# Performance work log

Measured on AMD Instinct MI355X. Metric: run time of the kernel, lower is better.

Reference implementation:

```python
import jax, jax.numpy as jnp
import numpy as np

C_IN = 128
C_HID = 32
N_HEADS = 4
INF = 1000000000.0


def setup_inputs() -> dict:
    key = jax.random.key(0)
    ks = jax.random.split(key, 12)
    B, I, J = 1, 256, 256
    hc = N_HEADS * C_HID
    s = 0.02
    return {
        "x": jax.random.normal(ks[0], (B, I, J, C_IN), dtype=jnp.float32),
        "mask": jnp.ones((B, I, J), dtype=jnp.float32),
        "ln_w": jnp.ones((C_IN,), dtype=jnp.float32),
        "ln_b": jnp.zeros((C_IN,), dtype=jnp.float32),
        "w_tri": jax.random.normal(ks[1], (C_IN, N_HEADS), dtype=jnp.float32) * s,
        "wq": jax.random.normal(ks[2], (C_IN, hc), dtype=jnp.float32) * s,
        "wk": jax.random.normal(ks[3], (C_IN, hc), dtype=jnp.float32) * s,
        "wv": jax.random.normal(ks[4], (C_IN, hc), dtype=jnp.float32) * s,
        "wg": jax.random.normal(ks[5], (C_IN, hc), dtype=jnp.float32) * s,
        "bg": jnp.ones((hc,), dtype=jnp.float32),
        "wo": jax.random.normal(ks[6], (hc, C_IN), dtype=jnp.float32) * s,
        "bo": jnp.zeros((C_IN,), dtype=jnp.float32),
    }


def _layer_norm(x, w, b, eps=1e-5):
    mu = jnp.mean(x, axis=-1, keepdims=True)
    var = jnp.var(x, axis=-1, keepdims=True)
    return (x - mu) * jax.lax.rsqrt(var + eps) * w + b


def _triangle_attention(x, mask, ln_w, ln_b, w_tri, wq, wk, wv, wg, bg, wo, bo):
    # starting=True: no transpose. x: [B, I, J, C]
    B, I, J, C = x.shape
    x = _layer_norm(x, ln_w, ln_b)
    # mask_bias: [B, I, 1, 1, J]
    mask_bias = (INF * (mask - 1.0))[..., :, None, None, :]
    # triangle_bias: linear(x) -> [B, I, J, H], permute (2,0,1) -> [B, H, I, J], unsqueeze -> [B, 1, H, I, J]
    tri = jnp.einsum("bijc,ch->bhij", x, w_tri)[:, None]  # [B, 1, H, I, J]
    # q/k/v: [B, I, H, J, Ch]
    def proj(w):
        return jnp.einsum("bijc,c(" + "" + ")->bijc", x, w) if False else (
            (x @ w).reshape(B, I, J, N_HEADS, C_HID).transpose(0, 1, 3, 2, 4))
    q = proj(wq) * (C_HID ** -0.5)
    k = proj(wk)
    v = proj(wv)
    # scores: [B, I, H, J, J]; biases broadcast over H (mask_bias) / I (tri over b,1 dim matches i? no)
    scores = jnp.einsum("bihqc,bihkc->bihqk", q, k)
    scores = scores + mask_bias + tri  # tri [B,1,H,I,J] broadcasts: i-dim aligns with query? matches torch broadcast [B,I,H,J,J]+[B,1,H,J,J]... wait tri is [B,1,H,I,J] with I==J so it broadcasts over the batch-of-rows dim
    a = jax.nn.softmax(scores, axis=-1)
    o = jnp.einsum("bihqk,bihkc->bihqc", a, v)  # [B, I, H, J, Ch]
    o = o.transpose(0, 1, 3, 2, 4).reshape(B, I, J, N_HEADS * C_HID)
    g = jax.nn.sigmoid(x @ wg + bg)
    o = o * g
    return o @ wo + bo  # [B, I, J, C]


def reference(x, mask, ln_w, ln_b, w_tri, wq, wk, wv, wg, bg, wo, bo):
    return _triangle_attention(x, mask, ln_w, ln_b, w_tri, wq, wk, wv, wg, bg, wo, bo)
```

## Files before the change

kernel.cpp:

```cpp
#include <hip/hip_runtime.h>


typedef __attribute__((ext_vector_type(4))) float f32x4;
typedef __attribute__((ext_vector_type(8))) short bf16x8;
#define MFMA16(a, b, c) __builtin_amdgcn_mfma_f32_16x16x32_bf16(a, b, c, 0, 0, 0)
#define LOG2E 1.4426950408889634f

__device__ __forceinline__ float bf2f(unsigned int u16) {
    return __uint_as_float(u16 << 16);
}
__device__ __forceinline__ unsigned int f2bf(float f) {
    unsigned int u = __float_as_uint(f);
    return (u + 0x7fffu + ((u >> 16) & 1u)) >> 16;
}
__device__ __forceinline__ unsigned int pack2(float a, float b) {
    return f2bf(a) | (f2bf(b) << 16);
}
__device__ __forceinline__ unsigned int cvt_pk_bf16(float lo, float hi) {
    unsigned int r;
    asm("v_cvt_pk_bf16_f32 %0, %1, %2" : "=v"(r) : "v"(lo), "v"(hi));
    return r;
}

__global__ __launch_bounds__(128) void k_prep(
    const float* __restrict__ wq, const float* __restrict__ wk,
    const float* __restrict__ wv, const float* __restrict__ wg,
    const float* __restrict__ wo, unsigned short* __restrict__ wT)
{
    const int mat = blockIdx.x, k0 = blockIdx.y * 16, t = threadIdx.x;
    const float* W = (mat == 0) ? wq : (mat == 1) ? wk : (mat == 2) ? wv
                     : (mat == 3) ? wg : wo;
    unsigned short* T = wT + mat * 16384;
    float col[16];
    #pragma unroll
    for (int kk = 0; kk < 16; ++kk) col[kk] = W[(k0 + kk) * 128 + t];
    unsigned int pk[8];
    #pragma unroll
    for (int u = 0; u < 8; ++u) pk[u] = pack2(col[2 * u], col[2 * u + 1]);
    *(uint4*)(T + t * 128 + k0)     = make_uint4(pk[0], pk[1], pk[2], pk[3]);
    *(uint4*)(T + t * 128 + k0 + 8) = make_uint4(pk[4], pk[5], pk[6], pk[7]);
}

__global__ __launch_bounds__(256, 2) void k_lnproj(
    const float* __restrict__ x, const float* __restrict__ ln_w,
    const float* __restrict__ ln_b, const float* __restrict__ w_tri,
    const unsigned short* __restrict__ wT, const float* __restrict__ bg,
    unsigned short* __restrict__ qb, unsigned short* __restrict__ kb,
    unsigned short* __restrict__ vtb, unsigned short* __restrict__ gb,
    float* __restrict__ triT)
{
    __shared__ unsigned short sA[128 * 136];
    __shared__ unsigned short sB[128 * 136];
    __shared__ unsigned short sWt[16 * 136];

    const int t = threadIdx.x, w = t >> 6, lane = t & 63;
    const int l15 = lane & 15, g = lane >> 4;
    const int rowBase = blockIdx.x * 128;

    if (t < 128) {
        const float4 wv = ((const float4*)w_tri)[t];
        sWt[0 * 136 + t] = (unsigned short)f2bf(wv.x);
        sWt[1 * 136 + t] = (unsigned short)f2bf(wv.y);
        sWt[2 * 136 + t] = (unsigned short)f2bf(wv.z);
        sWt[3 * 136 + t] = (unsigned short)f2bf(wv.w);
    } else {
        #pragma unroll
        for (int u = 0; u < 13; ++u) {
            const int idx = (t - 128) + 128 * u;
            if (idx < 12 * 136) sWt[4 * 136 + idx] = 0;
        }
    }

    {
        const int r = t >> 1, half = t & 1;
        const float* xr = x + (size_t)(rowBase + r) * 128 + half * 64;
        float v[64];
        float s1 = 0.0f, s2 = 0.0f;
        #pragma unroll
        for (int u = 0; u < 16; ++u) {
            const float4 q4 = ((const float4*)xr)[u];
            v[4*u] = q4.x; v[4*u+1] = q4.y; v[4*u+2] = q4.z; v[4*u+3] = q4.w;
            s1 += q4.x + q4.y + q4.z + q4.w;
            s2 += q4.x*q4.x + q4.y*q4.y + q4.z*q4.z + q4.w*q4.w;
        }
        s1 += __shfl_xor(s1, 1);
        s2 += __shfl_xor(s2, 1);
        const float mu = s1 * (1.0f / 128.0f);
        const float rs = rsqrtf(s2 * (1.0f / 128.0f) - mu * mu + 1e-5f);
        const float4* lw = (const float4*)(ln_w + half * 64);
        const float4* lb = (const float4*)(ln_b + half * 64);
        #pragma unroll
        for (int u = 0; u < 16; ++u) {
            const float4 w4 = lw[u], b4 = lb[u];
            v[4*u]   = (v[4*u]   - mu) * rs * w4.x + b4.x;
            v[4*u+1] = (v[4*u+1] - mu) * rs * w4.y + b4.y;
            v[4*u+2] = (v[4*u+2] - mu) * rs * w4.z + b4.z;
            v[4*u+3] = (v[4*u+3] - mu) * rs * w4.w + b4.w;
        }
        #pragma unroll
        for (int u = 0; u < 8; ++u) {
            uint4 pk;
            pk.x = pack2(v[8*u],   v[8*u+1]);
            pk.y = pack2(v[8*u+2], v[8*u+3]);
            pk.z = pack2(v[8*u+4], v[8*u+5]);
            pk.w = pack2(v[8*u+6], v[8*u+7]);
            *(uint4*)&sA[r * 136 + half * 64 + u * 8] = pk;
        }
    }
    __syncthreads();

    bf16x8 af[2][4];
    #pragma unroll
    for (int m = 0; m < 2; ++m)
        #pragma unroll
        for (int ks = 0; ks < 4; ++ks)
            af[m][ks] = *(const bf16x8*)&sA[(w * 32 + m * 16 + l15) * 136 + ks * 32 + g * 8];

    #pragma unroll
    for (int m = 0; m < 2; ++m) {
        f32x4 tc = (f32x4){0.f, 0.f, 0.f, 0.f};
        #pragma unroll
        for (int ks = 0; ks < 4; ++ks) {
            const bf16x8 bfw = *(const bf16x8*)&sWt[l15 * 136 + ks * 32 + g * 8];
            tc = MFMA16(af[m][ks], bfw, tc);
        }
        if (l15 < 4) {
            #pragma unroll
            for (int reg = 0; reg < 4; ++reg) {
                const int gr = rowBase + w * 32 + m * 16 + 4 * g + reg;
                triT[l15 * 65536 + gr] = tc[reg] * LOG2E;
            }
        }
    }

    const int r2 = t >> 1, half2 = t & 1;
    for (int mat = 0; mat < 4; ++mat) {
        {
            const unsigned short* Wm = wT + mat * 16384 + r2 * 128 + half2 * 64;
            #pragma unroll
            for (int u = 0; u < 8; ++u)
                *(uint4*)&sB[r2 * 136 + half2 * 64 + u * 8] = *(const uint4*)(Wm + u * 8);
        }
        __syncthreads();

        f32x4 acc[2][8];
        #pragma unroll
        for (int m = 0; m < 2; ++m)
            #pragma unroll
            for (int n = 0; n < 8; ++n) acc[m][n] = (f32x4){0.f, 0.f, 0.f, 0.f};
        #pragma unroll
        for (int n = 0; n < 8; ++n)
            #pragma unroll
            for (int ks = 0; ks < 4; ++ks) {
                const bf16x8 bf = *(const bf16x8*)&sB[(n * 16 + l15) * 136 + ks * 32 + g * 8];
                acc[0][n] = MFMA16(af[0][ks], bf, acc[0][n]);
                acc[1][n] = MFMA16(af[1][ks], bf, acc[1][n]);
            }
        __syncthreads();

        float bgv[8];
        if (mat == 3) {
            #pragma unroll
            for (int n = 0; n < 8; ++n) bgv[n] = bg[n * 16 + l15];
        }
        const float scl = (mat == 0) ? 0.25503486245f : 1.0f;
        #pragma unroll
        for (int m = 0; m < 2; ++m)
            #pragma unroll
            for (int n = 0; n < 8; ++n) {
                float vv[4];
                #pragma unroll
                for (int reg = 0; reg < 4; ++reg) {
                    float z = acc[m][n][reg];
                    if (mat == 3) z = 1.0f / (1.0f + __expf(-(z + bgv[n])));
                    else z *= scl;
                    vv[reg] = z;
                }
                const unsigned int a01 = cvt_pk_bf16(vv[0], vv[1]);
                const unsigned int a23 = cvt_pk_bf16(vv[2], vv[3]);
                const int qr = w * 32 + m * 16 + g * 4;
                const int col = n * 16 + l15;
                sB[qr * 136 + col]       = (unsigned short)a01;
                sB[(qr + 1) * 136 + col] = (unsigned short)(a01 >> 16);
                sB[(qr + 2) * 136 + col] = (unsigned short)a23;
                sB[(qr + 3) * 136 + col] = (unsigned short)(a23 >> 16);
            }
        __syncthreads();

        const int row = rowBase + r2;
        if (mat < 2) {
            unsigned short* dst = (mat == 0) ? qb : kb;
            const int i = row >> 8, j = row & 255;
            #pragma unroll
            for (int u = 0; u < 8; ++u) {
                const int c0 = half2 * 64 + u * 8;
                const int hh = c0 >> 5, ch = c0 & 31;
                *(uint4*)(dst + (((size_t)(i * 4 + hh)) * 256 + j) * 32 + ch) =
                    *(const uint4*)&sB[r2 * 136 + c0];
            }
        } else if (mat == 2) {
            const int c = t & 127, jh = t >> 7;
            const int i = rowBase >> 8;
            const int j0 = (rowBase & 255) + jh * 64;
            unsigned short buf[64];
            #pragma unroll
            for (int u = 0; u < 64; ++u) buf[u] = sB[(jh * 64 + u) * 136 + c];
            unsigned short* dst = vtb + ((size_t)(i * 128 + c)) * 256 + j0;
            #pragma unroll
            for (int u = 0; u < 8; ++u)
                *(uint4*)(dst + u * 8) = *(uint4*)&buf[u * 8];
        } else {
            #pragma unroll
            for (int u = 0; u < 8; ++u) {
                const int c0 = half2 * 64 + u * 8;
                *(uint4*)(gb + (size_t)row * 128 + c0) = *(const uint4*)&sB[r2 * 136 + c0];
            }
        }
        __syncthreads();
    }
}

__global__ __launch_bounds__(256, 3) void k_attn6(
    const unsigned short* __restrict__ qb, const unsigned short* __restrict__ kb,
    const unsigned short* __restrict__ vtb, const float* __restrict__ mask,
    const float* __restrict__ triT, const unsigned short* __restrict__ gb,
    unsigned short* __restrict__ ob)
{
    __shared__ unsigned short sK[256 * 32];
    __shared__ unsigned short sVt[32 * 260];
    __shared__ unsigned short sP[4][64 * 36];
    __shared__ float sM[256];

    const int i = blockIdx.x, h = blockIdx.y, t = threadIdx.x;
    const int w = t >> 6, lane = t & 63, l15 = lane & 15, g = lane >> 4;
    const size_t base = (size_t)(i * 4 + h) * 8192;

    {
        const uint4* ks = (const uint4*)(kb + base + t * 32);
        char* kdst = (char*)sK + t * 64;
        const int kswz = (t & 3) << 4;
        #pragma unroll
        for (int u = 0; u < 4; ++u)
            *(uint4*)(kdst + ((u * 16) ^ kswz)) = ks[u];

        const int ch = t >> 3, seg = t & 7;
        const uint4* vs = (const uint4*)(vtb + base + (size_t)ch * 256 + seg * 32);
        unsigned short* vdst = &sVt[ch * 260 + seg * 32];
        #pragma unroll
        for (int u = 0; u < 4; ++u)
            *(uint4*)(vdst + u * 8) = vs[u];

        sM[t] = (LOG2E * 1.0e9f) * (mask[i * 256 + t] - 1.0f);
    }

    const int q0 = w * 64;
    bf16x8 qf[4];
    #pragma unroll
    for (int m = 0; m < 4; ++m)
        qf[m] = *(const bf16x8*)(qb + base + (size_t)(q0 + m * 16 + l15) * 32 + g * 8);

    bf16x8 ones;
    #pragma unroll
    for (int u = 0; u < 8; ++u) ones[u] = (short)0x3F80;

    __syncthreads();

    f32x4 acc[4][2], accL[4];
    #pragma unroll
    for (int m = 0; m < 4; ++m) {
        acc[m][0] = (f32x4){0.f, 0.f, 0.f, 0.f};
        acc[m][1] = (f32x4){0.f, 0.f, 0.f, 0.f};
        accL[m]   = (f32x4){0.f, 0.f, 0.f, 0.f};
    }

    unsigned short* sPw = &sP[w][0];
    const float* triQ = triT + h * 65536;
    const f32x4 zero = (f32x4){0.f, 0.f, 0.f, 0.f};

    #pragma unroll
    for (int kt = 0; kt < 4; ++kt) {
        const int kv0 = kt * 64;
        #pragma unroll
        for (int hh = 0; hh < 2; ++hh) {
            const int kvh = kv0 + hh * 32;

            bf16x8 kf[2];
            #pragma unroll
            for (int n2 = 0; n2 < 2; ++n2) {
                const int row = kvh + n2 * 16 + l15;
                kf[n2] = *(const bf16x8*)((const char*)sK + row * 64 +
                                          ((g * 16) ^ ((row & 3) << 4)));
            }
            float4 mk[2];
            #pragma unroll
            for (int n2 = 0; n2 < 2; ++n2)
                mk[n2] = *(const float4*)&sM[kvh + n2 * 16 + g * 4];

            float4 tvb[2][2];
            #pragma unroll
            for (int n2 = 0; n2 < 2; ++n2)
                tvb[0][n2] = *(const float4*)
                    (triQ + (q0 + l15) * 256 + kvh + n2 * 16 + g * 4);

            #pragma unroll
            for (int m = 0; m < 4; ++m) {
                f32x4 p[2];
                #pragma unroll
                for (int n2 = 0; n2 < 2; ++n2)
                    p[n2] = MFMA16(kf[n2], qf[m], zero);
                if (m < 3) {
                    #pragma unroll
                    for (int n2 = 0; n2 < 2; ++n2)
                        tvb[(m + 1) & 1][n2] = *(const float4*)
                            (triQ + (q0 + (m + 1) * 16 + l15) * 256 + kvh + n2 * 16 + g * 4);
                }
                #pragma unroll
                for (int n2 = 0; n2 < 2; ++n2) {
                    const float4 tv = tvb[m & 1][n2];
                    p[n2][0] = exp2f(p[n2][0] + mk[n2].x + tv.x);
                    p[n2][1] = exp2f(p[n2][1] + mk[n2].y + tv.y);
                    p[n2][2] = exp2f(p[n2][2] + mk[n2].z + tv.z);
                    p[n2][3] = exp2f(p[n2][3] + mk[n2].w + tv.w);
                }
                #pragma unroll
                for (int n2 = 0; n2 < 2; ++n2) {
                    const unsigned int a01 = cvt_pk_bf16(p[n2][0], p[n2][1]);
                    const unsigned int a23 = cvt_pk_bf16(p[n2][2], p[n2][3]);
                    *(uint2*)&sPw[(m * 16 + l15) * 36 + n2 * 16 + g * 4] =
                        make_uint2(a01, a23);
                }
            }

            const bf16x8 vf0 = *(const bf16x8*)&sVt[l15 * 260 + kvh + g * 8];
            const bf16x8 vf1 = *(const bf16x8*)&sVt[(16 + l15) * 260 + kvh + g * 8];
            #pragma unroll
            for (int m = 0; m < 4; ++m) {
                const bf16x8 pb = *(const bf16x8*)&sPw[(m * 16 + l15) * 36 + g * 8];
                acc[m][0] = MFMA16(vf0, pb, acc[m][0]);
                acc[m][1] = MFMA16(vf1, pb, acc[m][1]);
                accL[m]   = MFMA16(ones, pb, accL[m]);
            }
        }
    }

    #pragma unroll
    for (int m = 0; m < 4; ++m) {
        const float inv = 1.0f / accL[m][0];
        const int q = q0 + m * 16 + l15;
        const unsigned short* gp = gb + (size_t)(i * 256 + q) * 128 + h * 32;
        unsigned short* op = ob + (((size_t)(i * 256 + q)) * 4 + h) * 32;
        #pragma unroll
        for (int n2 = 0; n2 < 2; ++n2) {
            const uint2 gv = *(const uint2*)(gp + n2 * 16 + g * 4);
            const float g0 = bf2f(gv.x & 0xffffu), g1 = bf2f(gv.x >> 16);
            const float g2 = bf2f(gv.y & 0xffffu), g3 = bf2f(gv.y >> 16);
            const unsigned int a01 =
                cvt_pk_bf16(acc[m][n2][0] * inv * g0, acc[m][n2][1] * inv * g1);
            const unsigned int a23 =
                cvt_pk_bf16(acc[m][n2][2] * inv * g2, acc[m][n2][3] * inv * g3);
            *(uint2*)(op + n2 * 16 + g * 4) = make_uint2(a01, a23);
        }
    }
}

__global__ __launch_bounds__(256, 3) void k_out3(
    const unsigned short* __restrict__ ob, const unsigned short* __restrict__ woT,
    const float* __restrict__ bo, float* __restrict__ out)
{
    __shared__ unsigned short sA[128 * 136];
    __shared__ unsigned short sB[128 * 72];
    const int t = threadIdx.x, w = t >> 6, lane = t & 63;
    const int l15 = lane & 15, g = lane >> 4;
    const int rowBase = blockIdx.x * 128;
    const int r = t >> 1, half = t & 1;

    #pragma unroll
    for (int u = 0; u < 8; ++u) {
        const int c = half * 64 + u * 8;
        *(uint4*)&sA[r * 136 + c] = *(const uint4*)(ob + (size_t)(rowBase + r) * 128 + c);
    }

    f32x4 acc[2][8];
    #pragma unroll
    for (int m = 0; m < 2; ++m)
        #pragma unroll
        for (int n = 0; n < 8; ++n) acc[m][n] = (f32x4){0.f, 0.f, 0.f, 0.f};

    #pragma unroll
    for (int kc = 0; kc < 2; ++kc) {
        #pragma unroll
        for (int u = 0; u < 4; ++u)
            *(uint4*)&sB[r * 72 + half * 32 + u * 8] =
                *(const uint4*)(woT + r * 128 + kc * 64 + half * 32 + u * 8);
        __syncthreads();
        #pragma unroll
        for (int ks = 0; ks < 2; ++ks) {
            const bf16x8 a0 = *(const bf16x8*)
                &sA[(w * 32 + l15) * 136 + kc * 64 + ks * 32 + g * 8];
            const bf16x8 a1 = *(const bf16x8*)
                &sA[(w * 32 + 16 + l15) * 136 + kc * 64 + ks * 32 + g * 8];
            #pragma unroll
            for (int n = 0; n < 8; ++n) {
                const bf16x8 bf = *(const bf16x8*)&sB[(n * 16 + l15) * 72 + ks * 32 + g * 8];
                acc[0][n] = MFMA16(a0, bf, acc[0][n]);
                acc[1][n] = MFMA16(a1, bf, acc[1][n]);
            }
        }
        __syncthreads();
    }

    float bov[8];
    #pragma unroll
    for (int n = 0; n < 8; ++n) bov[n] = bo[n * 16 + l15];
    #pragma unroll
    for (int m = 0; m < 2; ++m)
        #pragma unroll
        for (int n = 0; n < 8; ++n)
            #pragma unroll
            for (int reg = 0; reg < 4; ++reg) {
                const int row = rowBase + w * 32 + m * 16 + g * 4 + reg;
                out[(size_t)row * 128 + n * 16 + l15] = acc[m][n][reg] + bov[n];
            }
}

extern "C" void kernel_launch(void* const* d_in, const int* in_sizes, int n_in,
                              void* d_out, int out_size, void* d_ws, size_t ws_size,
                              hipStream_t stream) {
    (void)in_sizes; (void)n_in; (void)out_size; (void)ws_size;
    const float* x     = (const float*)d_in[0];
    const float* mask  = (const float*)d_in[1];
    const float* ln_w  = (const float*)d_in[2];
    const float* ln_b  = (const float*)d_in[3];
    const float* w_tri = (const float*)d_in[4];
    const float* wq    = (const float*)d_in[5];
    const float* wk    = (const float*)d_in[6];
    const float* wv    = (const float*)d_in[7];
    const float* wg    = (const float*)d_in[8];
    const float* bg    = (const float*)d_in[9];
    const float* wo    = (const float*)d_in[10];
    const float* bo    = (const float*)d_in[11];
    float* out = (float*)d_out;

    char* ws = (char*)d_ws;
    unsigned short* qb   = (unsigned short*)(ws + (16u << 20));
    unsigned short* kb   = (unsigned short*)(ws + (32u << 20));
    unsigned short* vtb  = (unsigned short*)(ws + (48u << 20));
    unsigned short* gb   = (unsigned short*)(ws + (64u << 20));
    unsigned short* ob   = (unsigned short*)(ws + (80u << 20));
    float*          triT = (float*)(ws + (96u << 20));
    unsigned short* wT   = (unsigned short*)(ws + (97u << 20));

    k_prep<<<dim3(5, 8), 128, 0, stream>>>(wq, wk, wv, wg, wo, wT);
    k_lnproj<<<512, 256, 0, stream>>>(x, ln_w, ln_b, w_tri, wT, bg,
                                      qb, kb, vtb, gb, triT);
    k_attn6<<<dim3(256, 4), 256, 0, stream>>>(qb, kb, vtb, mask, triT, gb, ob);
    k_out3<<<512, 256, 0, stream>>>(ob, wT + 4 * 16384, bo, out);
}
```

Before: 106.3 us.

## Store triangle bias in bf16, load V directly to registers, prefetch bias

The triangle bias is stored as bf16 instead of fp32, which halves its global traffic in the attention kernel. The V tile is no longer staged through shared memory and is read straight from global into registers each key tile. The bias for the next half-tile is now double-buffered in registers ahead of use. The PV MFMA block gets raised wave priority, and launch bounds go to four blocks per CU because shared memory use drops. The cost is bf16 rounding of the bias, more register pressure, and uncoalesced per-lane global V reads.

```diff
diff --git a/kernel.cpp b/kernel.cpp
--- a/kernel.cpp
+++ b/kernel.cpp
@@ -47,7 +47,7 @@
     const unsigned short* __restrict__ wT, const float* __restrict__ bg,
     unsigned short* __restrict__ qb, unsigned short* __restrict__ kb,
     unsigned short* __restrict__ vtb, unsigned short* __restrict__ gb,
-    float* __restrict__ triT)
+    unsigned short* __restrict__ triTb)
 {
     __shared__ unsigned short sA[128 * 136];
     __shared__ unsigned short sB[128 * 136];
@@ -128,7 +128,7 @@
             #pragma unroll
             for (int reg = 0; reg < 4; ++reg) {
                 const int gr = rowBase + w * 32 + m * 16 + 4 * g + reg;
-                triT[l15 * 65536 + gr] = tc[reg] * LOG2E;
+                triTb[l15 * 65536 + gr] = (unsigned short)f2bf(tc[reg] * LOG2E);
             }
         }
     }
@@ -220,14 +220,13 @@
     }
 }
 
-__global__ __launch_bounds__(256, 3) void k_attn6(
+__global__ __launch_bounds__(256, 4) void k_attn8(
     const unsigned short* __restrict__ qb, const unsigned short* __restrict__ kb,
     const unsigned short* __restrict__ vtb, const float* __restrict__ mask,
-    const float* __restrict__ triT, const unsigned short* __restrict__ gb,
+    const unsigned short* __restrict__ triTb, const unsigned short* __restrict__ gb,
     unsigned short* __restrict__ ob)
 {
     __shared__ unsigned short sK[256 * 32];
-    __shared__ unsigned short sVt[32 * 260];
     __shared__ unsigned short sP[4][64 * 36];
     __shared__ float sM[256];
 
@@ -242,14 +241,6 @@
         #pragma unroll
         for (int u = 0; u < 4; ++u)
             *(uint4*)(kdst + ((u * 16) ^ kswz)) = ks[u];
-
-        const int ch = t >> 3, seg = t & 7;
-        const uint4* vs = (const uint4*)(vtb + base + (size_t)ch * 256 + seg * 32);
-        unsigned short* vdst = &sVt[ch * 260 + seg * 32];
-        #pragma unroll
-        for (int u = 0; u < 4; ++u)
-            *(uint4*)(vdst + u * 8) = vs[u];
-
         sM[t] = (LOG2E * 1.0e9f) * (mask[i * 256 + t] - 1.0f);
     }
 
@@ -262,6 +253,15 @@
     bf16x8 ones;
     #pragma unroll
     for (int u = 0; u < 8; ++u) ones[u] = (short)0x3F80;
+
+    const unsigned short* triQ = triTb + h * 65536;
+    ushort4 tv[2][4][2];
+    #pragma unroll
+    for (int m = 0; m < 4; ++m)
+        #pragma unroll
+        for (int n2 = 0; n2 < 2; ++n2)
+            tv[0][m][n2] = *(const ushort4*)
+                (triQ + (q0 + m * 16 + l15) * 256 + n2 * 16 + g * 4);
 
     __syncthreads();
 
@@ -274,15 +274,34 @@
     }
 
     unsigned short* sPw = &sP[w][0];
-    const float* triQ = triT + h * 65536;
+    const unsigned short* vbase = vtb + base;
     const f32x4 zero = (f32x4){0.f, 0.f, 0.f, 0.f};
 
     #pragma unroll
     for (int kt = 0; kt < 4; ++kt) {
         const int kv0 = kt * 64;
+        bf16x8 vreg[4];
+        #pragma unroll
+        for (int hh = 0; hh < 2; ++hh) {
+            vreg[hh * 2]     = *(const bf16x8*)(vbase + (size_t)l15 * 256 + kv0 + hh * 32 + g * 8);
+            vreg[hh * 2 + 1] = *(const bf16x8*)(vbase + (size_t)(16 + l15) * 256 + kv0 + hh * 32 + g * 8);
+        }
+
         #pragma unroll
         for (int hh = 0; hh < 2; ++hh) {
             const int kvh = kv0 + hh * 32;
+            const int s = kt * 2 + hh;
+            const int ph = s & 1;
+
+            if (s < 7) {
+                const int nkvh = ((s + 1) >> 1) * 64 + ((s + 1) & 1) * 32;
+                #pragma unroll
+                for (int m = 0; m < 4; ++m)
+                    #pragma unroll
+                    for (int n2 = 0; n2 < 2; ++n2)
+                        tv[ph ^ 1][m][n2] = *(const ushort4*)
+                            (triQ + (q0 + m * 16 + l15) * 256 + nkvh + n2 * 16 + g * 4);
+            }
 
             bf16x8 kf[2];
             #pragma unroll
@@ -295,12 +314,6 @@
             #pragma unroll
             for (int n2 = 0; n2 < 2; ++n2)
                 mk[n2] = *(const float4*)&sM[kvh + n2 * 16 + g * 4];
-
-            float4 tvb[2][2];
-            #pragma unroll
-            for (int n2 = 0; n2 < 2; ++n2)
-                tvb[0][n2] = *(const float4*)
-                    (triQ + (q0 + l15) * 256 + kvh + n2 * 16 + g * 4);
 
             #pragma unroll
             for (int m = 0; m < 4; ++m) {
@@ -308,19 +321,13 @@
                 #pragma unroll
                 for (int n2 = 0; n2 < 2; ++n2)
                     p[n2] = MFMA16(kf[n2], qf[m], zero);
-                if (m < 3) {
-                    #pragma unroll
-                    for (int n2 = 0; n2 < 2; ++n2)
-                        tvb[(m + 1) & 1][n2] = *(const float4*)
-                            (triQ + (q0 + (m + 1) * 16 + l15) * 256 + kvh + n2 * 16 + g * 4);
-                }
                 #pragma unroll
                 for (int n2 = 0; n2 < 2; ++n2) {
-                    const float4 tv = tvb[m & 1][n2];
-                    p[n2][0] = exp2f(p[n2][0] + mk[n2].x + tv.x);
-                    p[n2][1] = exp2f(p[n2][1] + mk[n2].y + tv.y);
-                    p[n2][2] = exp2f(p[n2][2] + mk[n2].z + tv.z);
-                    p[n2][3] = exp2f(p[n2][3] + mk[n2].w + tv.w);
+                    const ushort4 tvc = tv[ph][m][n2];
+                    p[n2][0] = exp2f(p[n2][0] + mk[n2].x + bf2f(tvc.x));
+                    p[n2][1] = exp2f(p[n2][1] + mk[n2].y + bf2f(tvc.y));
+                    p[n2][2] = exp2f(p[n2][2] + mk[n2].z + bf2f(tvc.z));
+                    p[n2][3] = exp2f(p[n2][3] + mk[n2].w + bf2f(tvc.w));
                 }
                 #pragma unroll
                 for (int n2 = 0; n2 < 2; ++n2) {
@@ -331,8 +338,9 @@
                 }
             }
 
-            const bf16x8 vf0 = *(const bf16x8*)&sVt[l15 * 260 + kvh + g * 8];
-            const bf16x8 vf1 = *(const bf16x8*)&sVt[(16 + l15) * 260 + kvh + g * 8];
+            const bf16x8 vf0 = vreg[hh * 2];
+            const bf16x8 vf1 = vreg[hh * 2 + 1];
+            __builtin_amdgcn_s_setprio(1);
             #pragma unroll
             for (int m = 0; m < 4; ++m) {
                 const bf16x8 pb = *(const bf16x8*)&sPw[(m * 16 + l15) * 36 + g * 8];
@@ -340,6 +348,7 @@
                 acc[m][1] = MFMA16(vf1, pb, acc[m][1]);
                 accL[m]   = MFMA16(ones, pb, accL[m]);
             }
+            __builtin_amdgcn_s_setprio(0);
         }
     }
 
@@ -442,17 +451,17 @@
     float* out = (float*)d_out;
 
     char* ws = (char*)d_ws;
-    unsigned short* qb   = (unsigned short*)(ws + (16u << 20));
-    unsigned short* kb   = (unsigned short*)(ws + (32u << 20));
-    unsigned short* vtb  = (unsigned short*)(ws + (48u << 20));
-    unsigned short* gb   = (unsigned short*)(ws + (64u << 20));
-    unsigned short* ob   = (unsigned short*)(ws + (80u << 20));
-    float*          triT = (float*)(ws + (96u << 20));
-    unsigned short* wT   = (unsigned short*)(ws + (97u << 20));
+    unsigned short* qb    = (unsigned short*)(ws + (16u << 20));
+    unsigned short* kb    = (unsigned short*)(ws + (32u << 20));
+    unsigned short* vtb   = (unsigned short*)(ws + (48u << 20));
+    unsigned short* gb    = (unsigned short*)(ws + (64u << 20));
+    unsigned short* ob    = (unsigned short*)(ws + (80u << 20));
+    unsigned short* triTb = (unsigned short*)(ws + (96u << 20));
+    unsigned short* wT    = (unsigned short*)(ws + (97u << 20));
 
     k_prep<<<dim3(5, 8), 128, 0, stream>>>(wq, wk, wv, wg, wo, wT);
     k_lnproj<<<512, 256, 0, stream>>>(x, ln_w, ln_b, w_tri, wT, bg,
-                                      qb, kb, vtb, gb, triT);
-    k_attn6<<<dim3(256, 4), 256, 0, stream>>>(qb, kb, vtb, mask, triT, gb, ob);
+                                      qb, kb, vtb, gb, triTb);
+    k_attn8<<<dim3(256, 4), 256, 0, stream>>>(qb, kb, vtb, mask, triTb, gb, ob);
     k_out3<<<512, 256, 0, stream>>>(ob, wT + 4 * 16384, bo, out);
 }
```

Result: slower. 160.4 us (+50.8%).
